# Optimization experiments

Measured on AMD Instinct MI355X. Metric: run time of the kernel, lower is better.

Reference implementation:

```python
import jax, jax.numpy as jnp
import numpy as np

RES = (64, 64)
TEMP = 0.1  # forward default temp

def _mgrid(res):
    # matches torch.meshgrid(linspace(0, r-1, r)...) with default 'ij' indexing
    gs = jnp.meshgrid(*[jnp.arange(r, dtype=jnp.float32) for r in res], indexing='ij')
    return jnp.stack(gs, 0)  # [2, H, W]

def setup_inputs() -> dict:
    key = jax.random.key(0)
    k1, k2 = jax.random.split(key)
    x = jax.random.normal(k1, (8, 32, RES[0], RES[1]), dtype=jnp.float32)
    of = jax.random.normal(k2, (8, 2, RES[0], RES[1]), dtype=jnp.float32)
    return {"x": x, "of": of}

def reference(x, of):
    bs, C = x.shape[0], x.shape[1]
    hw = RES[0] * RES[1]
    gpos = _mgrid(RES).reshape(2, hw)                 # [2, HW] target pixel positions
    opos = gpos[None] + of.reshape(bs, 2, hw)         # [bs, 2, HW] flow-displaced source positions
    # L1 distance: logits[b, i, j] = sum_c |opos[b, c, j] - gpos[c, i]|
    dist = jnp.abs(opos[:, :, None, :] - gpos[None, :, :, None]).sum(axis=1)  # [bs, HW, HW]
    # softmax over target axis i (dim=-2 in torch) -> each source pixel j distributes mass over targets
    locs = jax.nn.softmax(-dist / TEMP, axis=1)       # [bs, HW, HW]
    # out[b, c, i] = sum_j x[b, c, j] * locs[b, i, j]
    out = jnp.einsum('bij,bcj->bci', locs, x.reshape(bs, C, hw))
    return out.reshape(bs, C, RES[0], RES[1])
```

## Files before the change

### kernel.cpp

```cpp
#include <hip/hip_runtime.h>
#include <math.h>

#define HW    4096
#define NC    32
#define NB    8
#define TINV  10.0f
#define RWIN  8
#define WDIM  (8 + 2 * RWIN)
#define RCUT  2.5f

__device__ __forceinline__ float readlane_f(float v, int l) {
    return __int_as_float(__builtin_amdgcn_readlane(__float_as_int(v), l));
}


__global__ __launch_bounds__(256) void prep_kernel(
    const float* __restrict__ x, const float* __restrict__ of,
    float4* __restrict__ params, float* __restrict__ xt)
{
    __shared__ float tile[32][257];
    int b  = blockIdx.x >> 4;
    int j0 = (blockIdx.x & 15) << 8;
    int t  = threadIdx.x;
    int j  = j0 + t;

    float oy = (float)(j >> 6) + of[(b * 2 + 0) * HW + j];
    float ox = (float)(j & 63) + of[(b * 2 + 1) * HW + j];

    int cy0 = min(max((int)floorf(oy), 0), 63);
    int cx0 = min(max((int)floorf(ox), 0), 63);
    float Dy = 0.f, Dx = 0.f;
    #pragma unroll
    for (int d = -3; d <= 3; ++d) {
        int iy = cy0 + d, ix = cx0 + d;
        if ((unsigned)iy < 64u) Dy += __expf(-TINV * fabsf(oy - (float)iy));
        if ((unsigned)ix < 64u) Dx += __expf(-TINV * fabsf(ox - (float)ix));
    }
    params[(b << 12) + j] = make_float4(oy, ox, 1.f / Dy, 1.f / Dx);

    #pragma unroll
    for (int c = 0; c < NC; ++c)
        tile[c][t] = x[((b * NC + c) << 12) + j];
    __syncthreads();
    #pragma unroll
    for (int k = 0; k < NC; ++k) {
        int o  = k * 256 + t;
        int jj = o >> 5, c = o & 31;
        xt[((size_t)((b << 12) + j0 + jj)) * NC + c] = tile[c][jj];
    }
}

__global__ __launch_bounds__(256) void gather_kernel(
    const float4* __restrict__ params, const float4* __restrict__ xt4,
    float* __restrict__ out)
{
    __shared__ float red[4 * 64 * 33];

    const int b    = blockIdx.y;
    const int tile = blockIdx.x;
    const int ty0  = (tile >> 3) << 3;
    const int tx0  = (tile & 7) << 3;

    const int lane = threadIdx.x & 63;
    const int wv   = __builtin_amdgcn_readfirstlane((int)(threadIdx.x >> 6));

    const float iy = (float)(ty0 + (lane >> 3));
    const float ix = (float)(tx0 + (lane & 7));

    float acc[NC];
    #pragma unroll
    for (int c = 0; c < NC; ++c) acc[c] = 0.f;

    const float4* pb = params + (b << 12);
    const float4* xb = xt4 + (size_t)(b << 12) * 8;

    const int srow = lane >> 5;
    const int scol = lane & 31;

    for (int r = 0; r < 3; ++r) {
        int ry = wv + srow * 4 + r * 8;
        int jy = ty0 - RWIN + ry;
        int jx = tx0 - RWIN + scol;
        bool valid = ((unsigned)jy < 64u) && ((unsigned)jx < 64u) && (scol < WDIM);
        int j = (jy << 6) + jx;
        float4 p = pb[valid ? j : 0];
        float cy = fminf(fmaxf(p.x, 0.f), 63.f);
        float cx = fminf(fmaxf(p.y, 0.f), 63.f);
        float dyr = fmaxf(fmaxf((float)ty0 - cy, cy - ((float)ty0 + 7.f)), 0.f);
        float dxr = fmaxf(fmaxf((float)tx0 - cx, cx - ((float)tx0 + 7.f)), 0.f);
        unsigned long long m = __ballot(valid && (dyr + dxr < RCUT));

        while (m) {
            int s0 = __builtin_ctzll(m); m &= m - 1;
            bool has1 = (m != 0ull);
            int s1 = has1 ? __builtin_ctzll(m) : s0;
            if (has1) m &= m - 1;

            int j0 = __builtin_amdgcn_readlane(j, s0);
            int j1 = __builtin_amdgcn_readlane(j, s1);
            const float4* x0 = xb + j0 * 8;
            const float4* x1 = xb + j1 * 8;
            float4 A[8], B[8];
            #pragma unroll
            for (int k = 0; k < 8; ++k) A[k] = x0[k];
            #pragma unroll
            for (int k = 0; k < 8; ++k) B[k] = x1[k];

            float w0, w1;
            {
                float soy = readlane_f(p.x, s0), sox = readlane_f(p.y, s0);
                float izy = readlane_f(p.z, s0), izx = readlane_f(p.w, s0);
                w0 = (__expf(-TINV * fabsf(soy - iy)) * izy)
                   * (__expf(-TINV * fabsf(sox - ix)) * izx);
            }
            {
                float soy = readlane_f(p.x, s1), sox = readlane_f(p.y, s1);
                float izy = readlane_f(p.z, s1), izx = readlane_f(p.w, s1);
                w1 = (__expf(-TINV * fabsf(soy - iy)) * izy)
                   * (__expf(-TINV * fabsf(sox - ix)) * izx);
                w1 = has1 ? w1 : 0.f;
            }

            #pragma unroll
            for (int k = 0; k < 8; ++k) {
                acc[4*k+0] = fmaf(w0, A[k].x, acc[4*k+0]);
                acc[4*k+1] = fmaf(w0, A[k].y, acc[4*k+1]);
                acc[4*k+2] = fmaf(w0, A[k].z, acc[4*k+2]);
                acc[4*k+3] = fmaf(w0, A[k].w, acc[4*k+3]);
            }
            #pragma unroll
            for (int k = 0; k < 8; ++k) {
                acc[4*k+0] = fmaf(w1, B[k].x, acc[4*k+0]);
                acc[4*k+1] = fmaf(w1, B[k].y, acc[4*k+1]);
                acc[4*k+2] = fmaf(w1, B[k].z, acc[4*k+2]);
                acc[4*k+3] = fmaf(w1, B[k].w, acc[4*k+3]);
            }
        }
    }

    float* myred = red + (wv * 64 + lane) * 33;
    #pragma unroll
    for (int c = 0; c < NC; ++c) myred[c] = acc[c];
    __syncthreads();

    int c  = threadIdx.x >> 3;
    int tg = threadIdx.x & 7;
    #pragma unroll
    for (int k = 0; k < 8; ++k) {
        int t = tg * 8 + k;
        float s = red[(0 * 64 + t) * 33 + c]
                + red[(1 * 64 + t) * 33 + c]
                + red[(2 * 64 + t) * 33 + c]
                + red[(3 * 64 + t) * 33 + c];
        out[(((b << 5) + c) << 12) + (ty0 + tg) * 64 + (tx0 + k)] = s;
    }
}

extern "C" void kernel_launch(void* const* d_in, const int* in_sizes, int n_in,
                              void* d_out, int out_size, void* d_ws, size_t ws_size,
                              hipStream_t stream) {
    const float* x  = (const float*)d_in[0];
    const float* of = (const float*)d_in[1];
    float* out = (float*)d_out;

    float4* params = (float4*)d_ws;
    float*  xt     = (float*)((char*)d_ws + NB * HW * sizeof(float4));

    prep_kernel<<<dim3(NB * 16), dim3(256), 0, stream>>>(x, of, params, xt);
    gather_kernel<<<dim3(64, NB), dim3(256), 0, stream>>>(params, (const float4*)xt, out);
}
```

Measured before the change: 74.69 us.

## Fuse prep into gather kernel with LDS-staged params and 4-way source batching

Removes the separate prep kernel and workspace transpose. Each block now computes the per-source flow parameters for its 24x24 window into LDS, then gathers x directly from the original channel-major layout using scalar strided loads. The inner loop processes four sources per iteration instead of two. The change avoids a kernel launch and a global round-trip for params and the transposed x. In exchange it recomputes window params redundantly across blocks and replaces contiguous float4 loads with 32 strided scalar loads per source.

```diff
diff --git a/kernel.cpp b/kernel.cpp
--- a/kernel.cpp
+++ b/kernel.cpp
@@ -7,63 +7,50 @@
 #define TINV  10.0f
 #define RWIN  8
 #define WDIM  (8 + 2 * RWIN)
+#define NSRC  (WDIM * WDIM)
 #define RCUT  2.5f
 
-__device__ __forceinline__ float readlane_f(float v, int l) {
-    return __int_as_float(__builtin_amdgcn_readlane(__float_as_int(v), l));
-}
-
-
-__global__ __launch_bounds__(256) void prep_kernel(
+__global__ __launch_bounds__(256) void fused_kernel(
     const float* __restrict__ x, const float* __restrict__ of,
-    float4* __restrict__ params, float* __restrict__ xt)
-{
-    __shared__ float tile[32][257];
-    int b  = blockIdx.x >> 4;
-    int j0 = (blockIdx.x & 15) << 8;
-    int t  = threadIdx.x;
-    int j  = j0 + t;
-
-    float oy = (float)(j >> 6) + of[(b * 2 + 0) * HW + j];
-    float ox = (float)(j & 63) + of[(b * 2 + 1) * HW + j];
-
-    int cy0 = min(max((int)floorf(oy), 0), 63);
-    int cx0 = min(max((int)floorf(ox), 0), 63);
-    float Dy = 0.f, Dx = 0.f;
-    #pragma unroll
-    for (int d = -3; d <= 3; ++d) {
-        int iy = cy0 + d, ix = cx0 + d;
-        if ((unsigned)iy < 64u) Dy += __expf(-TINV * fabsf(oy - (float)iy));
-        if ((unsigned)ix < 64u) Dx += __expf(-TINV * fabsf(ox - (float)ix));
-    }
-    params[(b << 12) + j] = make_float4(oy, ox, 1.f / Dy, 1.f / Dx);
-
-    #pragma unroll
-    for (int c = 0; c < NC; ++c)
-        tile[c][t] = x[((b * NC + c) << 12) + j];
-    __syncthreads();
-    #pragma unroll
-    for (int k = 0; k < NC; ++k) {
-        int o  = k * 256 + t;
-        int jj = o >> 5, c = o & 31;
-        xt[((size_t)((b << 12) + j0 + jj)) * NC + c] = tile[c][jj];
-    }
-}
-
-__global__ __launch_bounds__(256) void gather_kernel(
-    const float4* __restrict__ params, const float4* __restrict__ xt4,
     float* __restrict__ out)
 {
-    __shared__ float red[4 * 64 * 33];
+    __shared__ float4 plds[NSRC + 1];
+    __shared__ float  red[4 * 64 * 33];
 
     const int b    = blockIdx.y;
     const int tile = blockIdx.x;
     const int ty0  = (tile >> 3) << 3;
     const int tx0  = (tile & 7) << 3;
+    const int tid  = threadIdx.x;
 
-    const int lane = threadIdx.x & 63;
-    const int wv   = __builtin_amdgcn_readfirstlane((int)(threadIdx.x >> 6));
+    for (int s = tid; s < NSRC; s += 256) {
+        int sy = s / WDIM;
+        int sx = s - sy * WDIM;
+        int jy = ty0 - RWIN + sy;
+        int jx = tx0 - RWIN + sx;
+        float4 p = make_float4(0.f, 0.f, 0.f, 0.f);
+        if ((unsigned)jy < 64u && (unsigned)jx < 64u) {
+            int j = (jy << 6) + jx;
+            float oy = (float)jy + of[(b * 2 + 0) * HW + j];
+            float ox = (float)jx + of[(b * 2 + 1) * HW + j];
+            int cy0 = min(max((int)floorf(oy), 0), 63);
+            int cx0 = min(max((int)floorf(ox), 0), 63);
+            float Dy = 0.f, Dx = 0.f;
+            #pragma unroll
+            for (int d = -3; d <= 3; ++d) {
+                int iy = cy0 + d, ix = cx0 + d;
+                if ((unsigned)iy < 64u) Dy += __expf(-TINV * fabsf(oy - (float)iy));
+                if ((unsigned)ix < 64u) Dx += __expf(-TINV * fabsf(ox - (float)ix));
+            }
+            p = make_float4(oy, ox, 1.f / Dy, 1.f / Dx);
+        }
+        plds[s] = p;
+    }
+    if (tid == 0) plds[NSRC] = make_float4(0.f, 0.f, 0.f, 0.f);
+    __syncthreads();
 
+    const int lane = tid & 63;
+    const int wv   = __builtin_amdgcn_readfirstlane(tid >> 6);
     const float iy = (float)(ty0 + (lane >> 3));
     const float ix = (float)(tx0 + (lane & 7));
 
@@ -71,70 +58,87 @@
     #pragma unroll
     for (int c = 0; c < NC; ++c) acc[c] = 0.f;
 
-    const float4* pb = params + (b << 12);
-    const float4* xb = xt4 + (size_t)(b << 12) * 8;
-
     const int srow = lane >> 5;
     const int scol = lane & 31;
+    const float* xb = x + ((b * NC) << 12);
 
     for (int r = 0; r < 3; ++r) {
         int ry = wv + srow * 4 + r * 8;
-        int jy = ty0 - RWIN + ry;
-        int jx = tx0 - RWIN + scol;
-        bool valid = ((unsigned)jy < 64u) && ((unsigned)jx < 64u) && (scol < WDIM);
-        int j = (jy << 6) + jx;
-        float4 p = pb[valid ? j : 0];
+        bool lv = (scol < WDIM);
+        int  wi = ry * WDIM + scol;
+        float4 p = plds[lv ? wi : 0];
         float cy = fminf(fmaxf(p.x, 0.f), 63.f);
         float cx = fminf(fmaxf(p.y, 0.f), 63.f);
         float dyr = fmaxf(fmaxf((float)ty0 - cy, cy - ((float)ty0 + 7.f)), 0.f);
         float dxr = fmaxf(fmaxf((float)tx0 - cx, cx - ((float)tx0 + 7.f)), 0.f);
-        unsigned long long m = __ballot(valid && (dyr + dxr < RCUT));
+        unsigned long long m = __ballot(lv && (p.z != 0.f) && (dyr + dxr < RCUT));
 
         while (m) {
             int s0 = __builtin_ctzll(m); m &= m - 1;
-            bool has1 = (m != 0ull);
-            int s1 = has1 ? __builtin_ctzll(m) : s0;
-            if (has1) m &= m - 1;
+            int s1 = 64, s2 = 64, s3 = 64;
+            if (m) { s1 = __builtin_ctzll(m); m &= m - 1; }
+            if (m) { s2 = __builtin_ctzll(m); m &= m - 1; }
+            if (m) { s3 = __builtin_ctzll(m); m &= m - 1; }
 
-            int j0 = __builtin_amdgcn_readlane(j, s0);
-            int j1 = __builtin_amdgcn_readlane(j, s1);
-            const float4* x0 = xb + j0 * 8;
-            const float4* x1 = xb + j1 * 8;
-            float4 A[8], B[8];
-            #pragma unroll
-            for (int k = 0; k < 8; ++k) A[k] = x0[k];
-            #pragma unroll
-            for (int k = 0; k < 8; ++k) B[k] = x1[k];
-
-            float w0, w1;
+            int w0, w1i, w2i, w3i, j0, j1, j2, j3;
             {
-                float soy = readlane_f(p.x, s0), sox = readlane_f(p.y, s0);
-                float izy = readlane_f(p.z, s0), izx = readlane_f(p.w, s0);
-                w0 = (__expf(-TINV * fabsf(soy - iy)) * izy)
-                   * (__expf(-TINV * fabsf(sox - ix)) * izx);
+                int ry0 = wv + ((s0 >> 5) << 2) + (r << 3), rx0 = s0 & 31;
+                w0 = ry0 * WDIM + rx0;
+                j0 = ((ty0 - RWIN + ry0) << 6) + (tx0 - RWIN + rx0);
             }
             {
-                float soy = readlane_f(p.x, s1), sox = readlane_f(p.y, s1);
-                float izy = readlane_f(p.z, s1), izx = readlane_f(p.w, s1);
-                w1 = (__expf(-TINV * fabsf(soy - iy)) * izy)
-                   * (__expf(-TINV * fabsf(sox - ix)) * izx);
-                w1 = has1 ? w1 : 0.f;
+                int ry1 = wv + ((s1 >> 5) << 2) + (r << 3), rx1 = s1 & 31;
+                w1i = (s1 < 64) ? ry1 * WDIM + rx1 : NSRC;
+                j1  = (s1 < 64) ? ((ty0 - RWIN + ry1) << 6) + (tx0 - RWIN + rx1) : 0;
             }
+            {
+                int ry2 = wv + ((s2 >> 5) << 2) + (r << 3), rx2 = s2 & 31;
+                w2i = (s2 < 64) ? ry2 * WDIM + rx2 : NSRC;
+                j2  = (s2 < 64) ? ((ty0 - RWIN + ry2) << 6) + (tx0 - RWIN + rx2) : 0;
+            }
+            {
+                int ry3 = wv + ((s3 >> 5) << 2) + (r << 3), rx3 = s3 & 31;
+                w3i = (s3 < 64) ? ry3 * WDIM + rx3 : NSRC;
+                j3  = (s3 < 64) ? ((ty0 - RWIN + ry3) << 6) + (tx0 - RWIN + rx3) : 0;
+            }
+            j0 = __builtin_amdgcn_readfirstlane(j0);
+            j1 = __builtin_amdgcn_readfirstlane(j1);
+            j2 = __builtin_amdgcn_readfirstlane(j2);
+            j3 = __builtin_amdgcn_readfirstlane(j3);
+
+            float4 p0 = plds[w0], p1 = plds[w1i], p2 = plds[w2i], p3 = plds[w3i];
+            const float* x0 = xb + j0;
+            const float* x1 = xb + j1;
+            const float* x2 = xb + j2;
+            const float* x3 = xb + j3;
+
+            float A0[NC], A1[NC], A2[NC], A3[NC];
+            #pragma unroll
+            for (int k = 0; k < NC; ++k) A0[k] = x0[k << 12];
+            #pragma unroll
+            for (int k = 0; k < NC; ++k) A1[k] = x1[k << 12];
+            #pragma unroll
+            for (int k = 0; k < NC; ++k) A2[k] = x2[k << 12];
+            #pragma unroll
+            for (int k = 0; k < NC; ++k) A3[k] = x3[k << 12];
+
+            float g0 = (__expf(-TINV * fabsf(p0.x - iy)) * p0.z)
+                     * (__expf(-TINV * fabsf(p0.y - ix)) * p0.w);
+            float g1 = (__expf(-TINV * fabsf(p1.x - iy)) * p1.z)
+                     * (__expf(-TINV * fabsf(p1.y - ix)) * p1.w);
+            float g2 = (__expf(-TINV * fabsf(p2.x - iy)) * p2.z)
+                     * (__expf(-TINV * fabsf(p2.y - ix)) * p2.w);
+            float g3 = (__expf(-TINV * fabsf(p3.x - iy)) * p3.z)
+                     * (__expf(-TINV * fabsf(p3.y - ix)) * p3.w);
 
             #pragma unroll
-            for (int k = 0; k < 8; ++k) {
-                acc[4*k+0] = fmaf(w0, A[k].x, acc[4*k+0]);
-                acc[4*k+1] = fmaf(w0, A[k].y, acc[4*k+1]);
-                acc[4*k+2] = fmaf(w0, A[k].z, acc[4*k+2]);
-                acc[4*k+3] = fmaf(w0, A[k].w, acc[4*k+3]);
-            }
+            for (int c = 0; c < NC; ++c) acc[c] = fmaf(g0, A0[c], acc[c]);
             #pragma unroll
-            for (int k = 0; k < 8; ++k) {
-                acc[4*k+0] = fmaf(w1, B[k].x, acc[4*k+0]);
-                acc[4*k+1] = fmaf(w1, B[k].y, acc[4*k+1]);
-                acc[4*k+2] = fmaf(w1, B[k].z, acc[4*k+2]);
-                acc[4*k+3] = fmaf(w1, B[k].w, acc[4*k+3]);
-            }
+            for (int c = 0; c < NC; ++c) acc[c] = fmaf(g1, A1[c], acc[c]);
+            #pragma unroll
+            for (int c = 0; c < NC; ++c) acc[c] = fmaf(g2, A2[c], acc[c]);
+            #pragma unroll
+            for (int c = 0; c < NC; ++c) acc[c] = fmaf(g3, A3[c], acc[c]);
         }
     }
 
@@ -143,8 +147,8 @@
     for (int c = 0; c < NC; ++c) myred[c] = acc[c];
     __syncthreads();
 
-    int c  = threadIdx.x >> 3;
-    int tg = threadIdx.x & 7;
+    int c  = tid >> 3;
+    int tg = tid & 7;
     #pragma unroll
     for (int k = 0; k < 8; ++k) {
         int t = tg * 8 + k;
@@ -162,10 +166,7 @@
     const float* x  = (const float*)d_in[0];
     const float* of = (const float*)d_in[1];
     float* out = (float*)d_out;
+    (void)d_ws; (void)ws_size;
 
-    float4* params = (float4*)d_ws;
-    float*  xt     = (float*)((char*)d_ws + NB * HW * sizeof(float4));
-
-    prep_kernel<<<dim3(NB * 16), dim3(256), 0, stream>>>(x, of, params, xt);
-    gather_kernel<<<dim3(64, NB), dim3(256), 0, stream>>>(params, (const float4*)xt, out);
+    fused_kernel<<<dim3(64, NB), dim3(256), 0, stream>>>(x, of, out);
 }
```

Measured after the change: 89.92 us. 1.2x slower.

## Split gather channels across two blocks and compact active sources via LDS

Applied to the files above, without the earlier changes.

The gather grid gains a dimension that splits the 32 channels into two halves, doubling the block count (512 to 1024) and halving the accumulator registers per thread. Active source pixels are compacted into shared memory with mbcnt, and each wave now reads their params from LDS instead of using per-lane readlane. The inner loop also processes four sources per iteration instead of two. The cost is that weight computation and the window scan are repeated in both channel halves, and the kernel uses more LDS traffic.

```diff
diff --git a/kernel.cpp b/kernel.cpp
--- a/kernel.cpp
+++ b/kernel.cpp
@@ -8,10 +8,6 @@
 #define RWIN  8
 #define WDIM  (8 + 2 * RWIN)
 #define RCUT  2.5f
-
-__device__ __forceinline__ float readlane_f(float v, int l) {
-    return __int_as_float(__builtin_amdgcn_readlane(__float_as_int(v), l));
-}
 
 
 __global__ __launch_bounds__(256) void prep_kernel(
@@ -54,25 +50,29 @@
     const float4* __restrict__ params, const float4* __restrict__ xt4,
     float* __restrict__ out)
 {
-    __shared__ float red[4 * 64 * 33];
-
-    const int b    = blockIdx.y;
+    __shared__ float  red[4 * 64 * 17];
+    __shared__ float4 wp[4][64];
+    __shared__ int    sj[4][64];
+
+    const int b    = blockIdx.z;
+    const int h    = blockIdx.y;
     const int tile = blockIdx.x;
     const int ty0  = (tile >> 3) << 3;
     const int tx0  = (tile & 7) << 3;
 
-    const int lane = threadIdx.x & 63;
-    const int wv   = __builtin_amdgcn_readfirstlane((int)(threadIdx.x >> 6));
+    const int tid  = threadIdx.x;
+    const int lane = tid & 63;
+    const int wv   = __builtin_amdgcn_readfirstlane(tid >> 6);
 
     const float iy = (float)(ty0 + (lane >> 3));
     const float ix = (float)(tx0 + (lane & 7));
 
-    float acc[NC];
-    #pragma unroll
-    for (int c = 0; c < NC; ++c) acc[c] = 0.f;
+    float acc[16];
+    #pragma unroll
+    for (int c = 0; c < 16; ++c) acc[c] = 0.f;
 
     const float4* pb = params + (b << 12);
-    const float4* xb = xt4 + (size_t)(b << 12) * 8;
+    const float4* xb = xt4 + (size_t)(b << 12) * 8 + h * 4;
 
     const int srow = lane >> 5;
     const int scol = lane & 31;
@@ -88,71 +88,102 @@
         float cx = fminf(fmaxf(p.y, 0.f), 63.f);
         float dyr = fmaxf(fmaxf((float)ty0 - cy, cy - ((float)ty0 + 7.f)), 0.f);
         float dxr = fmaxf(fmaxf((float)tx0 - cx, cx - ((float)tx0 + 7.f)), 0.f);
-        unsigned long long m = __ballot(valid && (dyr + dxr < RCUT));
-
-        while (m) {
-            int s0 = __builtin_ctzll(m); m &= m - 1;
-            bool has1 = (m != 0ull);
-            int s1 = has1 ? __builtin_ctzll(m) : s0;
-            if (has1) m &= m - 1;
-
-            int j0 = __builtin_amdgcn_readlane(j, s0);
-            int j1 = __builtin_amdgcn_readlane(j, s1);
+        bool pred = valid && (dyr + dxr < RCUT);
+
+        unsigned long long m = __ballot(pred);
+        int cnt = __popcll(m);
+        if (pred) {
+            int pos = __builtin_amdgcn_mbcnt_hi((unsigned)(m >> 32),
+                      __builtin_amdgcn_mbcnt_lo((unsigned)m, 0u));
+            wp[wv][pos] = p;
+            sj[wv][pos] = j;
+        }
+
+        for (int k = 0; k < cnt; k += 4) {
+            int i0 = k;
+            int i1 = min(k + 1, cnt - 1);
+            int i2 = min(k + 2, cnt - 1);
+            int i3 = min(k + 3, cnt - 1);
+            float4 p0 = wp[wv][i0], p1 = wp[wv][i1];
+            float4 p2 = wp[wv][i2], p3 = wp[wv][i3];
+            int j0 = __builtin_amdgcn_readfirstlane(sj[wv][i0]);
+            int j1 = __builtin_amdgcn_readfirstlane(sj[wv][i1]);
+            int j2 = __builtin_amdgcn_readfirstlane(sj[wv][i2]);
+            int j3 = __builtin_amdgcn_readfirstlane(sj[wv][i3]);
+
             const float4* x0 = xb + j0 * 8;
             const float4* x1 = xb + j1 * 8;
-            float4 A[8], B[8];
-            #pragma unroll
-            for (int k = 0; k < 8; ++k) A[k] = x0[k];
-            #pragma unroll
-            for (int k = 0; k < 8; ++k) B[k] = x1[k];
-
-            float w0, w1;
-            {
-                float soy = readlane_f(p.x, s0), sox = readlane_f(p.y, s0);
-                float izy = readlane_f(p.z, s0), izx = readlane_f(p.w, s0);
-                w0 = (__expf(-TINV * fabsf(soy - iy)) * izy)
-                   * (__expf(-TINV * fabsf(sox - ix)) * izx);
-            }
-            {
-                float soy = readlane_f(p.x, s1), sox = readlane_f(p.y, s1);
-                float izy = readlane_f(p.z, s1), izx = readlane_f(p.w, s1);
-                w1 = (__expf(-TINV * fabsf(soy - iy)) * izy)
-                   * (__expf(-TINV * fabsf(sox - ix)) * izx);
-                w1 = has1 ? w1 : 0.f;
-            }
-
-            #pragma unroll
-            for (int k = 0; k < 8; ++k) {
-                acc[4*k+0] = fmaf(w0, A[k].x, acc[4*k+0]);
-                acc[4*k+1] = fmaf(w0, A[k].y, acc[4*k+1]);
-                acc[4*k+2] = fmaf(w0, A[k].z, acc[4*k+2]);
-                acc[4*k+3] = fmaf(w0, A[k].w, acc[4*k+3]);
-            }
-            #pragma unroll
-            for (int k = 0; k < 8; ++k) {
-                acc[4*k+0] = fmaf(w1, B[k].x, acc[4*k+0]);
-                acc[4*k+1] = fmaf(w1, B[k].y, acc[4*k+1]);
-                acc[4*k+2] = fmaf(w1, B[k].z, acc[4*k+2]);
-                acc[4*k+3] = fmaf(w1, B[k].w, acc[4*k+3]);
+            const float4* x2 = xb + j2 * 8;
+            const float4* x3 = xb + j3 * 8;
+            float4 A[4], B[4], C[4], D[4];
+            #pragma unroll
+            for (int u = 0; u < 4; ++u) A[u] = x0[u];
+            #pragma unroll
+            for (int u = 0; u < 4; ++u) B[u] = x1[u];
+            #pragma unroll
+            for (int u = 0; u < 4; ++u) C[u] = x2[u];
+            #pragma unroll
+            for (int u = 0; u < 4; ++u) D[u] = x3[u];
+
+            float g0 = (__expf(-TINV * fabsf(p0.x - iy)) * p0.z)
+                     * (__expf(-TINV * fabsf(p0.y - ix)) * p0.w);
+            float g1 = (__expf(-TINV * fabsf(p1.x - iy)) * p1.z)
+                     * (__expf(-TINV * fabsf(p1.y - ix)) * p1.w);
+            float g2 = (__expf(-TINV * fabsf(p2.x - iy)) * p2.z)
+                     * (__expf(-TINV * fabsf(p2.y - ix)) * p2.w);
+            float g3 = (__expf(-TINV * fabsf(p3.x - iy)) * p3.z)
+                     * (__expf(-TINV * fabsf(p3.y - ix)) * p3.w);
+            g1 = (k + 1 < cnt) ? g1 : 0.f;
+            g2 = (k + 2 < cnt) ? g2 : 0.f;
+            g3 = (k + 3 < cnt) ? g3 : 0.f;
+
+            #pragma unroll
+            for (int u = 0; u < 4; ++u) {
+                acc[4*u+0] = fmaf(g0, A[u].x, acc[4*u+0]);
+                acc[4*u+1] = fmaf(g0, A[u].y, acc[4*u+1]);
+                acc[4*u+2] = fmaf(g0, A[u].z, acc[4*u+2]);
+                acc[4*u+3] = fmaf(g0, A[u].w, acc[4*u+3]);
+            }
+            #pragma unroll
+            for (int u = 0; u < 4; ++u) {
+                acc[4*u+0] = fmaf(g1, B[u].x, acc[4*u+0]);
+                acc[4*u+1] = fmaf(g1, B[u].y, acc[4*u+1]);
+                acc[4*u+2] = fmaf(g1, B[u].z, acc[4*u+2]);
+                acc[4*u+3] = fmaf(g1, B[u].w, acc[4*u+3]);
+            }
+            #pragma unroll
+            for (int u = 0; u < 4; ++u) {
+                acc[4*u+0] = fmaf(g2, C[u].x, acc[4*u+0]);
+                acc[4*u+1] = fmaf(g2, C[u].y, acc[4*u+1]);
+                acc[4*u+2] = fmaf(g2, C[u].z, acc[4*u+2]);
+                acc[4*u+3] = fmaf(g2, C[u].w, acc[4*u+3]);
+            }
+            #pragma unroll
+            for (int u = 0; u < 4; ++u) {
+                acc[4*u+0] = fmaf(g3, D[u].x, acc[4*u+0]);
+                acc[4*u+1] = fmaf(g3, D[u].y, acc[4*u+1]);
+                acc[4*u+2] = fmaf(g3, D[u].z, acc[4*u+2]);
+                acc[4*u+3] = fmaf(g3, D[u].w, acc[4*u+3]);
             }
         }
     }
 
-    float* myred = red + (wv * 64 + lane) * 33;
-    #pragma unroll
-    for (int c = 0; c < NC; ++c) myred[c] = acc[c];
+    float* myred = red + (wv * 64 + lane) * 17;
+    #pragma unroll
+    for (int c = 0; c < 16; ++c) myred[c] = acc[c];
     __syncthreads();
 
-    int c  = threadIdx.x >> 3;
-    int tg = threadIdx.x & 7;
-    #pragma unroll
-    for (int k = 0; k < 8; ++k) {
-        int t = tg * 8 + k;
-        float s = red[(0 * 64 + t) * 33 + c]
-                + red[(1 * 64 + t) * 33 + c]
-                + red[(2 * 64 + t) * 33 + c]
-                + red[(3 * 64 + t) * 33 + c];
-        out[(((b << 5) + c) << 12) + (ty0 + tg) * 64 + (tx0 + k)] = s;
+    int c   = tid >> 4;
+    int t16 = tid & 15;
+    #pragma unroll
+    for (int k = 0; k < 4; ++k) {
+        int t = t16 + 16 * k;
+        float s = red[(0 * 64 + t) * 17 + c]
+                + red[(1 * 64 + t) * 17 + c]
+                + red[(2 * 64 + t) * 17 + c]
+                + red[(3 * 64 + t) * 17 + c];
+        int ch = h * 16 + c;
+        out[(((b << 5) + ch) << 12) + (ty0 + (t >> 3)) * 64 + (tx0 + (t & 7))] = s;
     }
 }
 
@@ -167,5 +198,5 @@
     float*  xt     = (float*)((char*)d_ws + NB * HW * sizeof(float4));
 
     prep_kernel<<<dim3(NB * 16), dim3(256), 0, stream>>>(x, of, params, xt);
-    gather_kernel<<<dim3(64, NB), dim3(256), 0, stream>>>(params, (const float4*)xt, out);
+    gather_kernel<<<dim3(64, 2, NB), dim3(256), 0, stream>>>(params, (const float4*)xt, out);
 }
```

New measurement: 74.64 us. No clear change (-0.1%).
